# Optimization experiments

Measured on AMD Instinct MI355X. Metric: run time of the kernel, lower is better.

The kernel has to match this reference:

```python
import jax, jax.numpy as jnp
import numpy as np

B, N, F = 2, 512, 128
NEG_SLOPE = 0.04
MASK_VAL = -9.0e15


def setup_inputs() -> dict:
    key = jax.random.key(0)
    ks = jax.random.split(key, 5)
    x = jax.random.normal(ks[0], (B, N, F), dtype=jnp.float32)
    adj = jax.random.randint(ks[1], (B, N, N), 0, 2, dtype=jnp.int32)
    s1 = 1.0 / np.sqrt(2 * F)
    # mlp(2F, [2F, 1], last_relu=False): Linear(2F,2F) -> ReLU -> Linear(2F,1)
    w1 = (jax.random.normal(ks[2], (2 * F, 2 * F), dtype=jnp.float32) * s1)
    b1 = jnp.zeros((2 * F,), dtype=jnp.float32)
    w2 = (jax.random.normal(ks[3], (1, 2 * F), dtype=jnp.float32) * s1)
    b2 = jnp.zeros((1,), dtype=jnp.float32)
    return {"x": x, "w1": w1, "b1": b1, "w2": w2, "b2": b2, "adj": adj}


def reference(x, w1, b1, w2, b2, adj):
    f = x.shape[-1]
    # concat(X_i, X_j) @ W1^T == X_i @ W1[:, :F]^T + X_j @ W1[:, F:]^T
    w1a, w1b = w1[:, :f], w1[:, f:]
    p = jnp.einsum('bnf,hf->bnh', x, w1a)          # [B,N,2F]  (i-part)
    q = jnp.einsum('bnf,hf->bnh', x, w1b)          # [B,N,2F]  (j-part)
    h = jax.nn.relu(p[:, :, None, :] + q[:, None, :, :] + b1)  # [B,N,N,2F]
    e = jnp.einsum('bijh,oh->bij', h, w2) + b2[0]  # [B,N,N] edge logits
    # LeakyReLU(negative_slope=0.04)
    e = jnp.where(e > 0, e, NEG_SLOPE * e)
    e = jnp.where(adj > 0, e, MASK_VAL)
    attention = jax.nn.softmax(e, axis=2)          # [B,N,N]
    next_h = jnp.einsum('bij,bjf->bif', attention, x)  # [B,N,F]
    return next_h, attention[0, 0, :]
```

## Files before the change

### kernel.cpp

```cpp
#include <hip/hip_runtime.h>

#define BB 2
#define NN 512
#define FF 128
#define HH 256
#define TI 4

__global__ __launch_bounds__(256) void k1_pq(const float* __restrict__ x,
    const float* __restrict__ w1, const float* __restrict__ b1,
    float* __restrict__ s_out, float* __restrict__ qT) {
  __shared__ __align__(16) float w1_l[64][FF];
  __shared__ float qtmp[64][17];
  const int t   = threadIdx.x;
  const int bn0 = blockIdx.x * 16;
  const int h0  = blockIdx.y * 64;
  const bool qh = (h0 >= HH);
  const int rowbase = qh ? (h0 - HH) : h0;
  const int colbase = qh ? FF : 0;

  #pragma unroll
  for (int k = 0; k < 8; ++k) {
    int idx = t + 256 * k;
    int r = idx >> 5, c4 = (idx & 31) * 4;
    float4 v = *(const float4*)(w1 + (rowbase + r) * (2 * FF) + colbase + c4);
    *(float4*)&w1_l[r][(c4 + 4 * r) & 127] = v;
  }
  __syncthreads();

  const int l  = t & 63;
  const int sb = __builtin_amdgcn_readfirstlane(t >> 6);
  const float* xr = x + (bn0 + sb * 4) * FF;
  float acc0 = 0.f, acc1 = 0.f, acc2 = 0.f, acc3 = 0.f;

  #pragma unroll 4
  for (int f4 = 0; f4 < FF; f4 += 4) {
    float4 wv = *(float4*)&w1_l[l][(f4 + 4 * l) & 127];
    float4 x0 = *(const float4*)(xr + f4);
    float4 x1 = *(const float4*)(xr + FF + f4);
    float4 x2 = *(const float4*)(xr + 2 * FF + f4);
    float4 x3 = *(const float4*)(xr + 3 * FF + f4);
    acc0 = fmaf(x0.x, wv.x, acc0); acc0 = fmaf(x0.y, wv.y, acc0);
    acc0 = fmaf(x0.z, wv.z, acc0); acc0 = fmaf(x0.w, wv.w, acc0);
    acc1 = fmaf(x1.x, wv.x, acc1); acc1 = fmaf(x1.y, wv.y, acc1);
    acc1 = fmaf(x1.z, wv.z, acc1); acc1 = fmaf(x1.w, wv.w, acc1);
    acc2 = fmaf(x2.x, wv.x, acc2); acc2 = fmaf(x2.y, wv.y, acc2);
    acc2 = fmaf(x2.z, wv.z, acc2); acc2 = fmaf(x2.w, wv.w, acc2);
    acc3 = fmaf(x3.x, wv.x, acc3); acc3 = fmaf(x3.y, wv.y, acc3);
    acc3 = fmaf(x3.z, wv.z, acc3); acc3 = fmaf(x3.w, wv.w, acc3);
  }

  const int bn = bn0 + sb * 4;
  if (!qh) {
    float bv = b1[h0 + l];
    s_out[(bn    ) * HH + h0 + l] = acc0 + bv;
    s_out[(bn + 1) * HH + h0 + l] = acc1 + bv;
    s_out[(bn + 2) * HH + h0 + l] = acc2 + bv;
    s_out[(bn + 3) * HH + h0 + l] = acc3 + bv;
  } else {
    qtmp[l][sb * 4]     = acc0;
    qtmp[l][sb * 4 + 1] = acc1;
    qtmp[l][sb * 4 + 2] = acc2;
    qtmp[l][sb * 4 + 3] = acc3;
    __syncthreads();
    #pragma unroll
    for (int k = 0; k < 4; ++k) {
      int idx = t + 256 * k;
      int r = idx >> 4, c = idx & 15;
      qT[(h0 - HH + r) * (BB * NN) + bn0 + c] = qtmp[r][c];
    }
  }
}

__global__ __launch_bounds__(1024) void k2_attn(const float* __restrict__ s,
    const float* __restrict__ qT, const float* __restrict__ x,
    const float* __restrict__ w2, const float* __restrict__ b2,
    const int* __restrict__ adj, float* __restrict__ out) {
  __shared__ __align__(16) float e_l[TI][NN];
  __shared__ __align__(16) float pe[2][TI][NN];
  __shared__ __align__(16) float part_l[4][TI][FF];
  __shared__ float red_m[TI][4];
  __shared__ float red_s[TI][4];

  const int blk = blockIdx.x;
  const int b   = blk >> 7;
  const int i0  = (blk & 127) * TI;
  const int t   = threadIdx.x;
  const int wv  = __builtin_amdgcn_readfirstlane(t >> 6);
  const int ln  = t & 63;

  {
    const int hg = wv >> 3;
    const int j  = (wv & 7) * 64 + ln;
    const float* qcol = qT + hg * 128 * (BB * NN) + b * NN + j;
    const float* s0   = s + (b * NN + i0) * HH + hg * 128;
    const float* w2p  = w2 + hg * 128;
    float a0 = 0.f, a1 = 0.f, a2 = 0.f, a3 = 0.f;
    #pragma unroll 8
    for (int h = 0; h < 128; ++h) {
      float qv = qcol[h * (BB * NN)];
      float wh = w2p[h];
      a0 = fmaf(fmaxf(s0[h]          + qv, 0.f), wh, a0);
      a1 = fmaf(fmaxf(s0[HH + h]     + qv, 0.f), wh, a1);
      a2 = fmaf(fmaxf(s0[2 * HH + h] + qv, 0.f), wh, a2);
      a3 = fmaf(fmaxf(s0[3 * HH + h] + qv, 0.f), wh, a3);
    }
    pe[hg][0][j] = a0; pe[hg][1][j] = a1;
    pe[hg][2][j] = a2; pe[hg][3][j] = a3;
  }
  __syncthreads();

  {
    const float b2v = b2[0];
    #pragma unroll
    for (int r = 0; r < 2; ++r) {
      int idx = t + 1024 * r;
      int ti = idx >> 9, j2 = idx & 511;
      float e = pe[0][ti][j2] + pe[1][ti][j2] + b2v;
      e = e > 0.f ? e : 0.04f * e;
      int av = adj[(b * NN + i0 + ti) * NN + j2];
      e_l[ti][j2] = (av > 0) ? e : -9.0e15f;
    }
  }
  __syncthreads();

  {
    const int ti = wv >> 2, qtr = wv & 3;
    float2 v = *(float2*)&e_l[ti][qtr * 128 + 2 * ln];
    float m = fmaxf(v.x, v.y);
    #pragma unroll
    for (int off = 32; off > 0; off >>= 1) m = fmaxf(m, __shfl_xor(m, off, 64));
    if (ln == 0) red_m[ti][qtr] = m;
    __syncthreads();
    m = fmaxf(fmaxf(red_m[ti][0], red_m[ti][1]), fmaxf(red_m[ti][2], red_m[ti][3]));
    v.x = __expf(v.x - m); v.y = __expf(v.y - m);
    float zs = v.x + v.y;
    #pragma unroll
    for (int off = 32; off > 0; off >>= 1) zs += __shfl_xor(zs, off, 64);
    if (ln == 0) red_s[ti][qtr] = zs;
    __syncthreads();
    float inv = 1.f / ((red_s[ti][0] + red_s[ti][1]) + (red_s[ti][2] + red_s[ti][3]));
    v.x *= inv; v.y *= inv;
    *(float2*)&e_l[ti][qtr * 128 + 2 * ln] = v;
  }
  __syncthreads();

  if (blk == 0 && t < NN) out[BB * NN * FF + t] = e_l[0][t];

  {
    const int ti = wv & 3, qtr = wv >> 2;
    const int jh = ln >> 5, fq = (ln & 31) * 4;
    const int jb = qtr * 128 + jh * 64;
    float4 acc = make_float4(0.f, 0.f, 0.f, 0.f);
    for (int s4 = 0; s4 < 16; ++s4) {
      const int j0 = jb + s4 * 4;
      float4 aa = *(float4*)&e_l[ti][j0];
      #pragma unroll
      for (int jj = 0; jj < 4; ++jj) {
        float4 xv = *(const float4*)(x + (b * NN + j0 + jj) * FF + fq);
        float w = (jj == 0) ? aa.x : (jj == 1) ? aa.y : (jj == 2) ? aa.z : aa.w;
        acc.x = fmaf(w, xv.x, acc.x);
        acc.y = fmaf(w, xv.y, acc.y);
        acc.z = fmaf(w, xv.z, acc.z);
        acc.w = fmaf(w, xv.w, acc.w);
      }
    }
    acc.x += __shfl_xor(acc.x, 32, 64);
    acc.y += __shfl_xor(acc.y, 32, 64);
    acc.z += __shfl_xor(acc.z, 32, 64);
    acc.w += __shfl_xor(acc.w, 32, 64);
    if (ln < 32) *(float4*)&part_l[qtr][ti][fq] = acc;
  }
  __syncthreads();
  if (t < TI * FF) {
    const int ti = t >> 7, f = t & 127;
    float r = (part_l[0][ti][f] + part_l[1][ti][f])
            + (part_l[2][ti][f] + part_l[3][ti][f]);
    out[(b * NN + i0 + ti) * FF + f] = r;
  }
}

extern "C" void kernel_launch(void* const* d_in, const int* in_sizes, int n_in,
                              void* d_out, int out_size, void* d_ws, size_t ws_size,
                              hipStream_t stream) {
  const float* x   = (const float*)d_in[0];
  const float* w1  = (const float*)d_in[1];
  const float* b1  = (const float*)d_in[2];
  const float* w2  = (const float*)d_in[3];
  const float* b2  = (const float*)d_in[4];
  const int*   adj = (const int*)  d_in[5];
  float* out = (float*)d_out;

  float* s  = (float*)d_ws;
  float* qT = s + BB * NN * HH;

  dim3 g1(BB * NN / 16, (2 * HH) / 64);
  k1_pq  <<<g1, 256, 0, stream>>>(x, w1, b1, s, qT);
  k2_attn<<<BB * NN / TI, 1024, 0, stream>>>(s, qT, x, w2, b2, adj, out);
}
```

Measured before the change: 93.32 us.

## Vectorize edge MLP and aggregation with packed float2 math and regrouped work

The edge-logit loop now splits the hidden dimension into four 64-wide groups, and each lane handles two adjacent j columns using packed v2f add, max and fma, which can map to packed FP32 instructions. The aggregation stage is reorganised so each wave covers 32 j values for all four rows, reusing each x load across the rows, with partial results reduced over 16 waves in shared memory. This aims to double per-instruction FP32 throughput and cut redundant x loads. The cost is more shared memory for partials and a longer final reduction.

```diff
diff --git a/kernel.cpp b/kernel.cpp
--- a/kernel.cpp
+++ b/kernel.cpp
@@ -5,6 +5,9 @@
 #define FF 128
 #define HH 256
 #define TI 4
+
+typedef float v2f __attribute__((ext_vector_type(2)));
+__device__ __forceinline__ v2f splat2(float s) { return (v2f){s, s}; }
 
 __global__ __launch_bounds__(256) void k1_pq(const float* __restrict__ x,
     const float* __restrict__ w1, const float* __restrict__ b1,
@@ -75,9 +78,9 @@
     const float* __restrict__ qT, const float* __restrict__ x,
     const float* __restrict__ w2, const float* __restrict__ b2,
     const int* __restrict__ adj, float* __restrict__ out) {
+  __shared__ __align__(16) float pe[4][TI][NN];
   __shared__ __align__(16) float e_l[TI][NN];
-  __shared__ __align__(16) float pe[2][TI][NN];
-  __shared__ __align__(16) float part_l[4][TI][FF];
+  __shared__ __align__(16) float part_l[16][TI][FF];
   __shared__ float red_m[TI][4];
   __shared__ float red_s[TI][4];
 
@@ -89,23 +92,31 @@
   const int ln  = t & 63;
 
   {
-    const int hg = wv >> 3;
-    const int j  = (wv & 7) * 64 + ln;
-    const float* qcol = qT + hg * 128 * (BB * NN) + b * NN + j;
-    const float* s0   = s + (b * NN + i0) * HH + hg * 128;
-    const float* w2p  = w2 + hg * 128;
-    float a0 = 0.f, a1 = 0.f, a2 = 0.f, a3 = 0.f;
+    const int hq = wv >> 2;
+    const int sl = wv & 3;
+    const int j0 = sl * 128 + 2 * ln;
+    const float* qp  = qT + hq * 64 * (BB * NN) + b * NN + j0;
+    const float* s0  = s + (b * NN + i0) * HH + hq * 64;
+    const float* w2p = w2 + hq * 64;
+    v2f a0 = {0.f, 0.f}, a1 = {0.f, 0.f}, a2 = {0.f, 0.f}, a3 = {0.f, 0.f};
     #pragma unroll 8
-    for (int h = 0; h < 128; ++h) {
-      float qv = qcol[h * (BB * NN)];
-      float wh = w2p[h];
-      a0 = fmaf(fmaxf(s0[h]          + qv, 0.f), wh, a0);
-      a1 = fmaf(fmaxf(s0[HH + h]     + qv, 0.f), wh, a1);
-      a2 = fmaf(fmaxf(s0[2 * HH + h] + qv, 0.f), wh, a2);
-      a3 = fmaf(fmaxf(s0[3 * HH + h] + qv, 0.f), wh, a3);
-    }
-    pe[hg][0][j] = a0; pe[hg][1][j] = a1;
-    pe[hg][2][j] = a2; pe[hg][3][j] = a3;
+    for (int h = 0; h < 64; ++h) {
+      v2f q2 = *(const v2f*)(qp + h * (BB * NN));
+      v2f w2v = splat2(w2p[h]);
+      v2f z = {0.f, 0.f};
+      v2f t0 = __builtin_elementwise_max(splat2(s0[h])           + q2, z);
+      v2f t1 = __builtin_elementwise_max(splat2(s0[HH + h])      + q2, z);
+      v2f t2 = __builtin_elementwise_max(splat2(s0[2 * HH + h])  + q2, z);
+      v2f t3 = __builtin_elementwise_max(splat2(s0[3 * HH + h])  + q2, z);
+      a0 = __builtin_elementwise_fma(t0, w2v, a0);
+      a1 = __builtin_elementwise_fma(t1, w2v, a1);
+      a2 = __builtin_elementwise_fma(t2, w2v, a2);
+      a3 = __builtin_elementwise_fma(t3, w2v, a3);
+    }
+    *(v2f*)&pe[hq][0][j0] = a0;
+    *(v2f*)&pe[hq][1][j0] = a1;
+    *(v2f*)&pe[hq][2][j0] = a2;
+    *(v2f*)&pe[hq][3][j0] = a3;
   }
   __syncthreads();
 
@@ -115,7 +126,7 @@
     for (int r = 0; r < 2; ++r) {
       int idx = t + 1024 * r;
       int ti = idx >> 9, j2 = idx & 511;
-      float e = pe[0][ti][j2] + pe[1][ti][j2] + b2v;
+      float e = (pe[0][ti][j2] + pe[1][ti][j2]) + (pe[2][ti][j2] + pe[3][ti][j2]) + b2v;
       e = e > 0.f ? e : 0.04f * e;
       int av = adj[(b * NN + i0 + ti) * NN + j2];
       e_l[ti][j2] = (av > 0) ? e : -9.0e15f;
@@ -147,34 +158,37 @@
   if (blk == 0 && t < NN) out[BB * NN * FF + t] = e_l[0][t];
 
   {
-    const int ti = wv & 3, qtr = wv >> 2;
-    const int jh = ln >> 5, fq = (ln & 31) * 4;
-    const int jb = qtr * 128 + jh * 64;
-    float4 acc = make_float4(0.f, 0.f, 0.f, 0.f);
-    for (int s4 = 0; s4 < 16; ++s4) {
-      const int j0 = jb + s4 * 4;
-      float4 aa = *(float4*)&e_l[ti][j0];
+    const int jb = wv * 32;
+    const int f2 = 2 * ln;
+    v2f acc[TI];
+    #pragma unroll
+    for (int ti = 0; ti < TI; ++ti) acc[ti] = (v2f){0.f, 0.f};
+
+    #pragma unroll 2
+    for (int g = 0; g < 8; ++g) {
+      const int j0 = jb + g * 4;
+      float4 aa[TI];
       #pragma unroll
-      for (int jj = 0; jj < 4; ++jj) {
-        float4 xv = *(const float4*)(x + (b * NN + j0 + jj) * FF + fq);
-        float w = (jj == 0) ? aa.x : (jj == 1) ? aa.y : (jj == 2) ? aa.z : aa.w;
-        acc.x = fmaf(w, xv.x, acc.x);
-        acc.y = fmaf(w, xv.y, acc.y);
-        acc.z = fmaf(w, xv.z, acc.z);
-        acc.w = fmaf(w, xv.w, acc.w);
+      for (int ti = 0; ti < TI; ++ti) aa[ti] = *(float4*)&e_l[ti][j0];
+      #pragma unroll
+      for (int k = 0; k < 4; ++k) {
+        v2f x2 = *(const v2f*)(x + (b * NN + j0 + k) * FF + f2);
+        #pragma unroll
+        for (int ti = 0; ti < TI; ++ti) {
+          float w = (k == 0) ? aa[ti].x : (k == 1) ? aa[ti].y : (k == 2) ? aa[ti].z : aa[ti].w;
+          acc[ti] = __builtin_elementwise_fma(splat2(w), x2, acc[ti]);
+        }
       }
     }
-    acc.x += __shfl_xor(acc.x, 32, 64);
-    acc.y += __shfl_xor(acc.y, 32, 64);
-    acc.z += __shfl_xor(acc.z, 32, 64);
-    acc.w += __shfl_xor(acc.w, 32, 64);
-    if (ln < 32) *(float4*)&part_l[qtr][ti][fq] = acc;
+    #pragma unroll
+    for (int ti = 0; ti < TI; ++ti) *(v2f*)&part_l[wv][ti][f2] = acc[ti];
   }
   __syncthreads();
   if (t < TI * FF) {
     const int ti = t >> 7, f = t & 127;
-    float r = (part_l[0][ti][f] + part_l[1][ti][f])
-            + (part_l[2][ti][f] + part_l[3][ti][f]);
+    float r = 0.f;
+    #pragma unroll
+    for (int w = 0; w < 16; ++w) r += part_l[w][ti][f];
     out[(b * NN + i0 + ti) * FF + f] = r;
   }
 }
```

Result: faster. 89.78 us (-3.8%).
